# Optimization experiments

Hardware: AMD Instinct MI355X
Metric: run time of the kernel (lower is better)

Reference implementation:

```python
import jax, jax.numpy as jnp
import numpy as np
from jax import lax


def _conv(x, w, b):
    # NCHW valid conv, stride 1 (torch Conv2d semantics)
    y = lax.conv_general_dilated(x, w, (1, 1), 'VALID',
                                 dimension_numbers=('NCHW', 'OIHW', 'NCHW'))
    return y + b[None, :, None, None]


def _maxpool(x, k, s):
    return lax.reduce_window(x, -jnp.inf, lax.max, (1, 1, k, k), (1, 1, s, s), 'VALID')


def _lin(x, w, b):
    # torch nn.Linear: y = x @ W^T + b, applied to last dim
    return x @ w.T + b


def setup_inputs() -> dict:
    key = jax.random.key(0)
    ks = jax.random.split(key, 21)
    def f(i, shape, scale):
        return jax.random.normal(ks[i], shape, dtype=jnp.float32) * scale
    return {
        'x': f(0, (512, 1, 28, 28), 1.0),
        'c1_w': f(1, (50, 1, 3, 3), 0.33), 'c1_b': f(2, (50,), 0.1),
        'c2_w': f(3, (50, 50, 3, 3), 0.047), 'c2_b': f(4, (50,), 0.05),
        'c3_w': f(5, (50, 50, 3, 3), 0.047), 'c3_b': f(6, (50,), 0.05),
        'l1_w': f(7, (500, 50), 0.14), 'l1_b': f(8, (500,), 0.05),
        'l2_w': f(9, (10, 500), 0.045), 'l2_b': f(10, (10,), 0.05),
        'd1_w': f(11, (3, 8450), 0.011), 'd1_b': f(12, (3,), 0.05),
        'd2_w': f(13, (2, 1250), 0.028), 'd2_b': f(14, (2,), 0.05),
        'c1c3_w': f(15, (13, 13), 0.28), 'c1c3_b': f(16, (13,), 0.05),
        'c1l1_w': f(17, (500, 1), 1.0), 'c1l1_b': f(18, (500,), 0.05),
        'c2l1_w': f(19, (500, 5), 0.45), 'c2l1_b': f(20, (500,), 0.05),
    }


def reference(x, c1_w, c1_b, c2_w, c2_b, c3_w, c3_b, l1_w, l1_b, l2_w, l2_b,
              d1_w, d1_b, d2_w, d2_b, c1c3_w, c1c3_b, c1l1_w, c1l1_b,
              c2l1_w, c2l1_b):
    B = x.shape[0]
    # stage 1: conv1 + relu + pool2 -> [B,50,13,13]
    h1 = _maxpool(jax.nn.relu(_conv(x, c1_w, c1_b)), 2, 2)
    # router 1 (argmax over 3 branches): 0 -> conv2 path, 1 -> c1_c3 path, 2 -> early-exit linear path
    d1 = jnp.argmax(_lin(h1.reshape(B, -1), d1_w, d1_b), axis=1)  # [B]
    # branch l11 (d1==2): pool7 -> [B,50,1,1], Linear(1->500) on last dim -> [B,50,1,500]
    l11 = _lin(_maxpool(h1, 7, 7), c1l1_w, c1l1_b)
    # branch c3-direct (d1==1): Linear(13->13) on last dim, then conv3+relu+pool2 -> [B,50,5,5]
    c33 = _lin(h1, c1c3_w, c1c3_b)
    c3d = _maxpool(jax.nn.relu(_conv(c33, c3_w, c3_b)), 2, 2)
    # branch c2 (d1==0): conv2+relu+pool2 -> [B,50,5,5]
    h2 = _maxpool(jax.nn.relu(_conv(h1, c2_w, c2_b)), 2, 2)
    # router 2 (argmax over 2 sub-branches)
    d2 = jnp.argmax(_lin(h2.reshape(B, -1), d2_w, d2_b), axis=1)  # [B]
    # sub-branch c32 (d2==0): conv3+relu+pool2 -> [B,50,1,1]
    c32 = _maxpool(jax.nn.relu(_conv(h2, c3_w, c3_b)), 2, 2)
    # sub-branch l12 (d2==1): Linear(5->500) on last dim -> [B,50,5,500], pool3 -> [B,50,1,166]
    l12 = _maxpool(_lin(h2, c2l1_w, c2l1_b), 3, 3)

    def head(t):
        # original: .view(-1, 50) -> linear1/relu/linear2/log_softmax; row-major flatten per sample
        r = t.reshape(B, -1, 50)
        return jax.nn.log_softmax(_lin(jax.nn.relu(_lin(r, l1_w, l1_b)), l2_w, l2_b), axis=-1)

    dt = x.dtype
    m_l11 = (d1 == 2).astype(dt)[:, None, None]
    m_c3d = (d1 == 1).astype(dt)[:, None, None]
    m_c32 = ((d1 == 0) & (d2 == 0)).astype(dt)[:, None, None]
    m_l12 = ((d1 == 0) & (d2 == 1)).astype(dt)[:, None, None]
    # dense masked combine (static-shape equivalent of the gather/compute/concat dispatch);
    # branch order matches the original concatenation: l11, l12, c32, c3-direct
    out = jnp.concatenate([head(l11) * m_l11, head(l12) * m_l12,
                           head(c32) * m_c32, head(c3d) * m_c3d], axis=1)  # [B,692,10]
    return out, d1, d2
```

## Files before the change

kernel.cpp:

```cpp
#include <hip/hip_runtime.h>
#include <hip/hip_bf16.h>
#include <math.h>

#define BB 512
#define CC 50

typedef __attribute__((ext_vector_type(8))) __bf16 bf16x8;
typedef __attribute__((ext_vector_type(4))) float f32x4;

__global__ void k_zero(float* __restrict__ out, int n4) {
  int i = blockIdx.x * 256 + threadIdx.x;
  if (i < n4) {
    float4 z = {0.f, 0.f, 0.f, 0.f};
    ((float4*)out)[i] = z;
  }
}

__global__ void k_pack(const float* __restrict__ l1w, const float* __restrict__ l1b,
                       const float* __restrict__ l2w,
                       __bf16* __restrict__ W1p, __bf16* __restrict__ W2p) {
  int idx = blockIdx.x * 256 + threadIdx.x;
  if (idx < 512 * 64) {
    int j = idx >> 6, k = idx & 63;
    float v = 0.f;
    if (j < 500) {
      if (k < 50) v = l1w[j * 50 + k];
      else if (k == 50) v = l1b[j];
    }
    W1p[idx] = (__bf16)v;
  } else if (idx < 512 * 64 + 16 * 512) {
    int i2 = idx - 512 * 64;
    int n = i2 >> 9, k2 = i2 & 511;
    float v = (n < 10 && k2 < 500) ? l2w[n * 500 + k2] : 0.f;
    W2p[i2] = (__bf16)v;
  }
}

__global__ void k_conv1(const float* __restrict__ x, const float* __restrict__ w,
                        const float* __restrict__ bias, float* __restrict__ h1) {
  int idx = blockIdx.x * 256 + threadIdx.x;
  if (idx >= BB * CC * 169) return;
  int b = idx / (CC * 169);
  int rem = idx % (CC * 169);
  int c = rem / 169;
  int p = rem % 169;
  int py = p / 13, px = p % 13;
  const float* xi = x + b * 784;
  float wr[9];
#pragma unroll
  for (int i = 0; i < 9; i++) wr[i] = w[c * 9 + i];
  float m = -INFINITY;
#pragma unroll
  for (int dy = 0; dy < 2; dy++)
#pragma unroll
    for (int dx = 0; dx < 2; dx++) {
      int y0 = 2 * py + dy, x0 = 2 * px + dx;
      float s = 0.f;
#pragma unroll
      for (int ky = 0; ky < 3; ky++)
#pragma unroll
        for (int kx = 0; kx < 3; kx++)
          s += xi[(y0 + ky) * 28 + x0 + kx] * wr[ky * 3 + kx];
      m = fmaxf(m, s);
    }
  h1[idx] = fmaxf(m + bias[c], 0.f);
}

__global__ void k_d1p7(const float* __restrict__ h1, const float* __restrict__ w,
                       const float* __restrict__ bias, int* __restrict__ d1i,
                       float* __restrict__ outd1, float* __restrict__ p7) {
  int b = blockIdx.x, t = threadIdx.x;
  const float* hb = h1 + b * 8450;
  float s0 = 0.f, s1 = 0.f, s2 = 0.f;
  for (int i = t; i < 8450; i += 256) {
    float v = hb[i];
    s0 += v * w[i];
    s1 += v * w[8450 + i];
    s2 += v * w[16900 + i];
  }
#pragma unroll
  for (int off = 32; off >= 1; off >>= 1) {
    s0 += __shfl_down(s0, off);
    s1 += __shfl_down(s1, off);
    s2 += __shfl_down(s2, off);
  }
  __shared__ float red[4][3];
  if ((t & 63) == 0) { red[t >> 6][0] = s0; red[t >> 6][1] = s1; red[t >> 6][2] = s2; }
  __syncthreads();
  if (t == 0) {
    float l0 = bias[0], l1v = bias[1], l2v = bias[2];
    for (int wv = 0; wv < 4; wv++) { l0 += red[wv][0]; l1v += red[wv][1]; l2v += red[wv][2]; }
    int idx = 0; float best = l0;
    if (l1v > best) { best = l1v; idx = 1; }
    if (l2v > best) { best = l2v; idx = 2; }
    d1i[b] = idx;
    outd1[b] = (float)idx;
  }
  if (t < 50) {
    const float* hp = hb + t * 169;
    float m = -INFINITY;
#pragma unroll
    for (int y = 0; y < 7; y++)
#pragma unroll
      for (int x = 0; x < 7; x++) m = fmaxf(m, hp[y * 13 + x]);
    p7[b * 50 + t] = m;
  }
}

template <int MODE>
__global__ __launch_bounds__(256) void k_conv5(const float* __restrict__ in,
                                               const float* __restrict__ w,
                                               const float* __restrict__ bias,
                                               const int* __restrict__ d1i,
                                               const float* __restrict__ w13,
                                               const float* __restrict__ b13,
                                               float* __restrict__ out) {
  int b = blockIdx.x;
  if (MODE == 1 && d1i[b] != 1) return;
  __shared__ float sh[50 * 260];
  __shared__ float w13s[182];
  int t = threadIdx.x;
  for (int i = t; i < 8450; i += 256) {
    int ic = i / 169, r = i % 169;
    int row = r / 13, xx = r % 13;
    sh[ic * 260 + row * 20 + xx] = in[b * 8450 + i];
  }
  if (MODE == 1) {
    for (int i = t; i < 182; i += 256) w13s[i] = (i < 169) ? w13[i] : b13[i - 169];
  }
  __syncthreads();
  if (MODE == 1) {
    for (int p = t; p < 650; p += 256) {
      float* row = sh + (p / 13) * 260 + (p % 13) * 20;
      float r[13];
#pragma unroll
      for (int k = 0; k < 13; k++) r[k] = row[k];
#pragma unroll
      for (int xx = 0; xx < 13; xx++) {
        float s = w13s[169 + xx];
#pragma unroll
        for (int k = 0; k < 13; k++) s += r[k] * w13s[xx * 13 + k];
        row[xx] = s;
      }
    }
    __syncthreads();
  }
  if (t >= 250) return;
  int oc = t / 5, py = t % 5;
  float acc[5][4];
#pragma unroll
  for (int i = 0; i < 5; i++)
#pragma unroll
    for (int j = 0; j < 4; j++) acc[i][j] = 0.f;
  const float* wb = w + oc * 450;
  for (int ic = 0; ic < 50; ic++) {
    float wv[9];
#pragma unroll
    for (int i = 0; i < 9; i++) wv[i] = wb[ic * 9 + i];
    float r[4][13];
    const float* rp = sh + ic * 260 + 2 * py * 20;
#pragma unroll
    for (int rr = 0; rr < 4; rr++) {
      const float* p4 = rp + rr * 20;
      float4 q0 = *(const float4*)(p4);
      float4 q1 = *(const float4*)(p4 + 4);
      float4 q2 = *(const float4*)(p4 + 8);
      r[rr][0] = q0.x; r[rr][1] = q0.y; r[rr][2] = q0.z; r[rr][3] = q0.w;
      r[rr][4] = q1.x; r[rr][5] = q1.y; r[rr][6] = q1.z; r[rr][7] = q1.w;
      r[rr][8] = q2.x; r[rr][9] = q2.y; r[rr][10] = q2.z; r[rr][11] = q2.w;
      r[rr][12] = p4[12];
    }
#pragma unroll
    for (int px = 0; px < 5; px++)
#pragma unroll
      for (int dy = 0; dy < 2; dy++)
#pragma unroll
        for (int dx = 0; dx < 2; dx++) {
          float s = acc[px][dy * 2 + dx];
          int x0 = 2 * px + dx;
#pragma unroll
          for (int ky = 0; ky < 3; ky++)
#pragma unroll
            for (int kx = 0; kx < 3; kx++)
              s += r[dy + ky][x0 + kx] * wv[ky * 3 + kx];
          acc[px][dy * 2 + dx] = s;
        }
  }
  float bs = bias[oc];
#pragma unroll
  for (int px = 0; px < 5; px++) {
    float m = fmaxf(fmaxf(acc[px][0], acc[px][1]), fmaxf(acc[px][2], acc[px][3]));
    out[((b * 50 + oc) * 5 + py) * 5 + px] = fmaxf(m + bs, 0.f);
  }
}

__global__ __launch_bounds__(256) void k_d2c(const float* __restrict__ h2,
                                             const float* __restrict__ d2w,
                                             const float* __restrict__ d2b,
                                             const float* __restrict__ c3w,
                                             const float* __restrict__ c3b,
                                             const float* __restrict__ c2l1w,
                                             const float* __restrict__ c2l1b,
                                             const int* __restrict__ d1i,
                                             int* __restrict__ d2i,
                                             float* __restrict__ outd2,
                                             float* __restrict__ c32,
                                             float* __restrict__ l12) {
  int b = blockIdx.x, t = threadIdx.x;
  __shared__ float hs[1250];
  __shared__ float wls[2500];
  __shared__ float bls[500];
  __shared__ float red[4][2];
  __shared__ int sd2;
  for (int i = t; i < 1250; i += 256) hs[i] = h2[b * 1250 + i];
  __syncthreads();
  float s0 = 0.f, s1 = 0.f;
  for (int i = t; i < 1250; i += 256) {
    float v = hs[i];
    s0 += v * d2w[i];
    s1 += v * d2w[1250 + i];
  }
#pragma unroll
  for (int off = 32; off >= 1; off >>= 1) {
    s0 += __shfl_down(s0, off);
    s1 += __shfl_down(s1, off);
  }
  if ((t & 63) == 0) { red[t >> 6][0] = s0; red[t >> 6][1] = s1; }
  __syncthreads();
  if (t == 0) {
    float l0 = d2b[0] + red[0][0] + red[1][0] + red[2][0] + red[3][0];
    float l1v = d2b[1] + red[0][1] + red[1][1] + red[2][1] + red[3][1];
    int idx = (l1v > l0) ? 1 : 0;
    d2i[b] = idx;
    outd2[b] = (float)idx;
    sd2 = idx;
  }
  __syncthreads();
  int d2v = sd2;
  if (d1i[b] != 0) return;
  if (d2v == 0) {
    if (t < 50) {
      const float* wb = c3w + t * 450;
      float a[4] = {0.f, 0.f, 0.f, 0.f};
      for (int ic = 0; ic < 50; ic++) {
        float r[4][4];
#pragma unroll
        for (int y = 0; y < 4; y++)
#pragma unroll
          for (int xx = 0; xx < 4; xx++) r[y][xx] = hs[ic * 25 + y * 5 + xx];
        float wv[9];
#pragma unroll
        for (int i = 0; i < 9; i++) wv[i] = wb[ic * 9 + i];
#pragma unroll
        for (int py = 0; py < 2; py++)
#pragma unroll
          for (int px = 0; px < 2; px++) {
            float s = a[py * 2 + px];
#pragma unroll
            for (int ky = 0; ky < 3; ky++)
#pragma unroll
              for (int kx = 0; kx < 3; kx++)
                s += r[py + ky][px + kx] * wv[ky * 3 + kx];
            a[py * 2 + px] = s;
          }
      }
      float m = fmaxf(fmaxf(a[0], a[1]), fmaxf(a[2], a[3]));
      c32[b * 50 + t] = fmaxf(m + c3b[t], 0.f);
    }
  } else {
    for (int i = t; i < 2500; i += 256) wls[i] = c2l1w[i];
    for (int i = t; i < 500; i += 256) bls[i] = c2l1b[i];
    __syncthreads();
    for (int o = t; o < 8300; o += 256) {
      int c = o / 166, tt = o % 166;
      const float* hb = hs + c * 25;
      float m = -INFINITY;
#pragma unroll
      for (int i = 0; i < 3; i++) {
        float a0 = hb[i * 5 + 0], a1 = hb[i * 5 + 1], a2 = hb[i * 5 + 2],
              a3 = hb[i * 5 + 3], a4 = hb[i * 5 + 4];
#pragma unroll
        for (int dj = 0; dj < 3; dj++) {
          int j = 3 * tt + dj;
          const float* wj = wls + j * 5;
          float s = bls[j] + a0 * wj[0] + a1 * wj[1] + a2 * wj[2] + a3 * wj[3] + a4 * wj[4];
          m = fmaxf(m, s);
        }
      }
      l12[b * 8300 + o] = m;
    }
  }
}

__device__ __forceinline__ int swz(int byteoff) {
  return byteoff ^ (((byteoff >> 7) & 7) << 4);
}

__global__ __launch_bounds__(256) void k_head(
    const float* __restrict__ h2, const float* __restrict__ c3d,
    const float* __restrict__ c32, const float* __restrict__ p7,
    const float* __restrict__ l12buf,
    const int* __restrict__ d1i, const int* __restrict__ d2i,
    const __bf16* __restrict__ W1p, const __bf16* __restrict__ W2p,
    const float* __restrict__ l2b,
    const float* __restrict__ c1l1w, const float* __restrict__ c1l1b,
    float* __restrict__ out) {
  int b = blockIdx.x >> 1;
  int half = blockIdx.x & 1;
  int d1 = d1i[b], d2 = d2i[b];
  int branch, nrows, rstart;
  if (d1 == 2)      { branch = 0; nrows = 500; rstart = 0; }
  else if (d1 == 1) { branch = 3; nrows = 25;  rstart = 667; }
  else if (d2 == 1) { branch = 1; nrows = 166; rstart = 500; }
  else              { branch = 2; nrows = 1;   rstart = 666; }
  int base = half * 256;
  if (base >= nrows) return;
  int nr = nrows - base; if (nr > 256) nr = 256;

  __shared__ __align__(16) char smem[53248];
  __bf16* Vs = (__bf16*)smem;
  char* Wst = smem;
  __bf16* Ht = (__bf16*)(smem + 32768);
  int t = threadIdx.x;

  for (int idx = t; idx < 256 * 64; idx += 256) {
    int row = idx >> 6, col = idx & 63;
    float val = 0.f;
    if (col == 50) val = 1.0f;
    else if (col < 50 && row < nr) {
      int rr = base + row;
      if (branch == 0) {
        int c = rr / 10; int j = (rr % 10) * 50 + col;
        val = p7[b * 50 + c] * c1l1w[j] + c1l1b[j];
      } else if (branch == 1) {
        val = l12buf[b * 8300 + rr * 50 + col];
      } else if (branch == 2) {
        val = c32[b * 50 + col];
      } else {
        int k = rr * 50 + col; int c = k / 25, s5 = k % 25;
        val = c3d[(b * 50 + c) * 25 + s5];
      }
    }
    Vs[row * 72 + col] = (__bf16)val;
  }

  bf16x8 st[4];
  {
    const __bf16* s0 = W1p + t * 32;
#pragma unroll
    for (int i = 0; i < 4; ++i) st[i] = *(const bf16x8*)(s0 + i * 8);
  }
  __syncthreads();

  int wv = t >> 6, lane = t & 63;
  int lr = lane & 15, lg = lane >> 4;
  int wbase = wv * 64;
  bool active = wbase < nr;
  int wrem = active ? (nr - wbase) : 0;
  int nmt = (wrem + 15) >> 4; if (nmt > 4) nmt = 4;

  bf16x8 a1[4][2];
  if (active) {
#pragma unroll
    for (int mt = 0; mt < 4; ++mt) {
      if (mt < nmt) {
#pragma unroll
        for (int ks = 0; ks < 2; ++ks)
          a1[mt][ks] = *(const bf16x8*)(Vs + (wbase + mt * 16 + lr) * 72 + ks * 32 + lg * 8);
      }
    }
  }
  __syncthreads();

  {
#pragma unroll
    for (int i = 0; i < 4; ++i)
      *(bf16x8*)(Wst + swz(t * 64 + i * 16)) = st[i];
  }
  __syncthreads();

  const __bf16* w2b = W2p + lr * 512 + lg * 8;
  f32x4 acc2[4];
#pragma unroll
  for (int mt = 0; mt < 4; ++mt) acc2[mt] = (f32x4){0.f, 0.f, 0.f, 0.f};
  bf16x8 b2n = *(const bf16x8*)(w2b);

  for (int c = 0; c < 4; ++c) {
    if (c < 3) {
      const __bf16* s2 = W1p + (c + 1) * 8192 + t * 32;
#pragma unroll
      for (int i = 0; i < 4; ++i) st[i] = *(const bf16x8*)(s2 + i * 8);
    }
    char* wb = Wst + (c & 1) * 16384;
    if (active) {
#pragma unroll
      for (int ql = 0; ql < 4; ++ql) {
        int q = c * 4 + ql;
        int boff = ql * 4096 + lr * 128 + lg * 16;
        bf16x8 bA0 = *(const bf16x8*)(wb + swz(boff));
        bf16x8 bA1 = *(const bf16x8*)(wb + swz(boff + 64));
        bf16x8 bB0 = *(const bf16x8*)(wb + swz(boff + 2048));
        bf16x8 bB1 = *(const bf16x8*)(wb + swz(boff + 2048 + 64));
#pragma unroll
        for (int mt = 0; mt < 4; ++mt) {
          if (mt < nmt) {
            f32x4 dz = {0.f, 0.f, 0.f, 0.f};
            f32x4 d = __builtin_amdgcn_mfma_f32_16x16x32_bf16(a1[mt][0], bA0, dz, 0, 0, 0);
            d = __builtin_amdgcn_mfma_f32_16x16x32_bf16(a1[mt][1], bA1, d, 0, 0, 0);
            __bf16* hp = Ht + (wv * 4 + mt) * 640;
#pragma unroll
            for (int r = 0; r < 4; ++r)
              hp[(lg * 4 + r) * 40 + lr] = (__bf16)fmaxf(d[r], 0.f);
          }
        }
#pragma unroll
        for (int mt = 0; mt < 4; ++mt) {
          if (mt < nmt) {
            f32x4 dz = {0.f, 0.f, 0.f, 0.f};
            f32x4 d = __builtin_amdgcn_mfma_f32_16x16x32_bf16(a1[mt][0], bB0, dz, 0, 0, 0);
            d = __builtin_amdgcn_mfma_f32_16x16x32_bf16(a1[mt][1], bB1, d, 0, 0, 0);
            __bf16* hp = Ht + (wv * 4 + mt) * 640;
#pragma unroll
            for (int r = 0; r < 4; ++r)
              hp[(lg * 4 + r) * 40 + 16 + lr] = (__bf16)fmaxf(d[r], 0.f);
          }
        }
        {
          bf16x8 bb2 = b2n;
          if (q < 15) b2n = *(const bf16x8*)(w2b + (q + 1) * 32);
#pragma unroll
          for (int mt = 0; mt < 4; ++mt) {
            if (mt < nmt) {
              bf16x8 a2 = *(const bf16x8*)(Ht + (wv * 4 + mt) * 640 + lr * 40 + lg * 8);
              acc2[mt] = __builtin_amdgcn_mfma_f32_16x16x32_bf16(a2, bb2, acc2[mt], 0, 0, 0);
            }
          }
        }
      }
    }
    if (c < 3) {
      char* wd = Wst + (1 - (c & 1)) * 16384;
#pragma unroll
      for (int i = 0; i < 4; ++i)
        *(bf16x8*)(wd + swz(t * 64 + i * 16)) = st[i];
    }
    __syncthreads();
  }
  if (!active) return;

  float bl = (lr < 10) ? l2b[lr] : 0.f;
#pragma unroll
  for (int mt = 0; mt < 4; ++mt) {
    if (mt < nmt) {
      float o[4], m[4], s[4];
#pragma unroll
      for (int r = 0; r < 4; ++r) {
        o[r] = acc2[mt][r] + bl;
        m[r] = (lr < 10) ? o[r] : -INFINITY;
      }
#pragma unroll
      for (int mk = 1; mk < 16; mk <<= 1)
#pragma unroll
        for (int r = 0; r < 4; ++r) m[r] = fmaxf(m[r], __shfl_xor(m[r], mk));
#pragma unroll
      for (int r = 0; r < 4; ++r) s[r] = (lr < 10) ? expf(o[r] - m[r]) : 0.f;
#pragma unroll
      for (int mk = 1; mk < 16; mk <<= 1)
#pragma unroll
        for (int r = 0; r < 4; ++r) s[r] += __shfl_xor(s[r], mk);
      if (lr < 10) {
#pragma unroll
        for (int r = 0; r < 4; ++r) {
          int rloc = wbase + mt * 16 + lg * 4 + r;
          if (rloc < nr)
            out[(b * 692 + rstart + base + rloc) * 10 + lr] = o[r] - (m[r] + logf(s[r]));
        }
      }
    }
  }
}

extern "C" void kernel_launch(void* const* d_in, const int* in_sizes, int n_in,
                              void* d_out, int out_size, void* d_ws, size_t ws_size,
                              hipStream_t stream) {
  const float* x     = (const float*)d_in[0];
  const float* c1w   = (const float*)d_in[1];
  const float* c1b   = (const float*)d_in[2];
  const float* c2w   = (const float*)d_in[3];
  const float* c2b   = (const float*)d_in[4];
  const float* c3w   = (const float*)d_in[5];
  const float* c3b   = (const float*)d_in[6];
  const float* l1w   = (const float*)d_in[7];
  const float* l1b   = (const float*)d_in[8];
  const float* l2w   = (const float*)d_in[9];
  const float* l2b   = (const float*)d_in[10];
  const float* d1w   = (const float*)d_in[11];
  const float* d1b   = (const float*)d_in[12];
  const float* d2w   = (const float*)d_in[13];
  const float* d2b   = (const float*)d_in[14];
  const float* c13w  = (const float*)d_in[15];
  const float* c13b  = (const float*)d_in[16];
  const float* c1l1w = (const float*)d_in[17];
  const float* c1l1b = (const float*)d_in[18];
  const float* c2l1w = (const float*)d_in[19];
  const float* c2l1b = (const float*)d_in[20];
  float* out = (float*)d_out;

  float* ws  = (float*)d_ws;
  float* h1  = ws;
  float* h2  = h1 + 4326400;
  float* c3d = h2 + 640000;
  float* c32 = c3d + 640000;
  float* p7  = c32 + 25600;
  int*   d1i = (int*)(p7 + 25600);
  int*   d2i = d1i + 512;
  __bf16* W1p = (__bf16*)(d2i + 512);
  __bf16* W2p = W1p + 512 * 64;
  float* l12buf = h1;

  float* outd1 = out + 512 * 692 * 10;
  float* outd2 = outd1 + 512;

  k_zero<<<3460, 256, 0, stream>>>(out, 885510);
  k_pack<<<160, 256, 0, stream>>>(l1w, l1b, l2w, W1p, W2p);
  k_conv1<<<16900, 256, 0, stream>>>(x, c1w, c1b, h1);
  k_d1p7<<<512, 256, 0, stream>>>(h1, d1w, d1b, d1i, outd1, p7);
  k_conv5<0><<<512, 256, 0, stream>>>(h1, c2w, c2b, d1i, c13w, c13b, h2);
  k_conv5<1><<<512, 256, 0, stream>>>(h1, c3w, c3b, d1i, c13w, c13b, c3d);
  k_d2c<<<512, 256, 0, stream>>>(h2, d2w, d2b, c3w, c3b, c2l1w, c2l1b,
                                 d1i, d2i, outd2, c32, l12buf);
  k_head<<<1024, 256, 0, stream>>>(h2, c3d, c32, p7, l12buf, d1i, d2i,
                                   W1p, W2p, l2b, c1l1w, c1l1b, out);
}
```

Before: 237.2 us.

## Replace LDS-staged head GEMM with register-only MFMA plus scalar FP32 second layer

The head kernel no longer stages activations and W1 tiles through shared memory with barriers and swizzling. Each wave loads its A fragments directly from global memory and streams W1 fragments from global/L2 with a two-deep register prefetch. The second linear layer (500->10) is now done as FP32 FMAs against a transposed W2 table, followed by a cross-lane shuffle reduction. The grid is split into four 128-row slabs per sample instead of two 256-row halves, so waves with no rows exit early. This removes LDS traffic and synchronization but adds many VALU FMAs, a large register accumulator array (80 floats), and 40 shuffle reductions per row tile.

```diff
diff --git a/kernel.cpp b/kernel.cpp
--- a/kernel.cpp
+++ b/kernel.cpp
@@ -18,7 +18,7 @@
 
 __global__ void k_pack(const float* __restrict__ l1w, const float* __restrict__ l1b,
                        const float* __restrict__ l2w,
-                       __bf16* __restrict__ W1p, __bf16* __restrict__ W2p) {
+                       __bf16* __restrict__ W1p, float* __restrict__ W2t) {
   int idx = blockIdx.x * 256 + threadIdx.x;
   if (idx < 512 * 64) {
     int j = idx >> 6, k = idx & 63;
@@ -28,11 +28,10 @@
       else if (k == 50) v = l1b[j];
     }
     W1p[idx] = (__bf16)v;
-  } else if (idx < 512 * 64 + 16 * 512) {
+  } else if (idx < 512 * 64 + 512 * 12) {
     int i2 = idx - 512 * 64;
-    int n = i2 >> 9, k2 = i2 & 511;
-    float v = (n < 10 && k2 < 500) ? l2w[n * 500 + k2] : 0.f;
-    W2p[i2] = (__bf16)v;
+    int j = i2 / 12, n = i2 % 12;
+    W2t[i2] = (n < 10 && j < 500) ? l2w[n * 500 + j] : 0.f;
   }
 }
 
@@ -292,188 +291,172 @@
   }
 }
 
-__device__ __forceinline__ int swz(int byteoff) {
-  return byteoff ^ (((byteoff >> 7) & 7) << 4);
-}
-
-__global__ __launch_bounds__(256) void k_head(
-    const float* __restrict__ h2, const float* __restrict__ c3d,
-    const float* __restrict__ c32, const float* __restrict__ p7,
-    const float* __restrict__ l12buf,
+__global__ __launch_bounds__(256) void k_gemm(
+    const float* __restrict__ c3d, const float* __restrict__ c32,
+    const float* __restrict__ p7, const float* __restrict__ l12buf,
     const int* __restrict__ d1i, const int* __restrict__ d2i,
-    const __bf16* __restrict__ W1p, const __bf16* __restrict__ W2p,
+    const __bf16* __restrict__ W1p, const float* __restrict__ W2t,
     const float* __restrict__ l2b,
     const float* __restrict__ c1l1w, const float* __restrict__ c1l1b,
     float* __restrict__ out) {
-  int b = blockIdx.x >> 1;
-  int half = blockIdx.x & 1;
+  int b = blockIdx.x >> 2;
+  int slab = blockIdx.x & 3;
   int d1 = d1i[b], d2 = d2i[b];
   int branch, nrows, rstart;
   if (d1 == 2)      { branch = 0; nrows = 500; rstart = 0; }
   else if (d1 == 1) { branch = 3; nrows = 25;  rstart = 667; }
   else if (d2 == 1) { branch = 1; nrows = 166; rstart = 500; }
   else              { branch = 2; nrows = 1;   rstart = 666; }
-  int base = half * 256;
-  if (base >= nrows) return;
-  int nr = nrows - base; if (nr > 256) nr = 256;
-
-  __shared__ __align__(16) char smem[53248];
-  __bf16* Vs = (__bf16*)smem;
-  char* Wst = smem;
-  __bf16* Ht = (__bf16*)(smem + 32768);
+
   int t = threadIdx.x;
-
-  for (int idx = t; idx < 256 * 64; idx += 256) {
-    int row = idx >> 6, col = idx & 63;
-    float val = 0.f;
-    if (col == 50) val = 1.0f;
-    else if (col < 50 && row < nr) {
-      int rr = base + row;
-      if (branch == 0) {
-        int c = rr / 10; int j = (rr % 10) * 50 + col;
-        val = p7[b * 50 + c] * c1l1w[j] + c1l1b[j];
-      } else if (branch == 1) {
-        val = l12buf[b * 8300 + rr * 50 + col];
-      } else if (branch == 2) {
-        val = c32[b * 50 + col];
-      } else {
-        int k = rr * 50 + col; int c = k / 25, s5 = k % 25;
-        val = c3d[(b * 50 + c) * 25 + s5];
-      }
-    }
-    Vs[row * 72 + col] = (__bf16)val;
-  }
-
-  bf16x8 st[4];
-  {
-    const __bf16* s0 = W1p + t * 32;
-#pragma unroll
-    for (int i = 0; i < 4; ++i) st[i] = *(const bf16x8*)(s0 + i * 8);
-  }
-  __syncthreads();
-
   int wv = t >> 6, lane = t & 63;
   int lr = lane & 15, lg = lane >> 4;
-  int wbase = wv * 64;
-  bool active = wbase < nr;
-  int wrem = active ? (nr - wbase) : 0;
-  int nmt = (wrem + 15) >> 4; if (nmt > 4) nmt = 4;
-
-  bf16x8 a1[4][2];
-  if (active) {
-#pragma unroll
-    for (int mt = 0; mt < 4; ++mt) {
+  int rowbase = slab * 128 + wv * 32;
+  if (rowbase >= nrows) return;
+  int rem = nrows - rowbase;
+  int nmt = (rem + 15) >> 4; if (nmt > 2) nmt = 2;
+
+  bf16x8 a1[2][2];
+#pragma unroll
+  for (int mt = 0; mt < 2; ++mt) {
+    int m = rowbase + mt * 16 + lr;
+    const float* src;
+    float p7v = 0.f; const float* wsrc = nullptr; const float* bsrc = nullptr;
+    if (branch == 0) {
+      p7v = p7[b * 50 + m / 10];
+      wsrc = c1l1w + (m % 10) * 50;
+      bsrc = c1l1b + (m % 10) * 50;
+      src = wsrc;
+    } else if (branch == 1) {
+      src = l12buf + b * 8300 + m * 50;
+    } else if (branch == 2) {
+      src = c32 + b * 50 + m * 50;
+    } else {
+      src = c3d + b * 1250 + m * 50;
+    }
+#pragma unroll
+    for (int ks = 0; ks < 2; ++ks) {
+      float v[8];
+      int k0 = ks * 32 + lg * 8;
+      if (ks == 0 || lg < 2) {
+        if (branch == 0) {
+#pragma unroll
+          for (int i = 0; i < 8; i += 2) {
+            float2 wq = *(const float2*)(wsrc + k0 + i);
+            float2 bq = *(const float2*)(bsrc + k0 + i);
+            v[i] = p7v * wq.x + bq.x;
+            v[i + 1] = p7v * wq.y + bq.y;
+          }
+        } else {
+#pragma unroll
+          for (int i = 0; i < 8; i += 2) {
+            float2 q = *(const float2*)(src + k0 + i);
+            v[i] = q.x; v[i + 1] = q.y;
+          }
+        }
+      } else if (lg == 2) {
+        float2 q;
+        if (branch == 0) {
+          float2 wq = *(const float2*)(wsrc + 48);
+          float2 bq = *(const float2*)(bsrc + 48);
+          q.x = p7v * wq.x + bq.x; q.y = p7v * wq.y + bq.y;
+        } else {
+          q = *(const float2*)(src + 48);
+        }
+        v[0] = q.x; v[1] = q.y; v[2] = 1.0f;
+        v[3] = 0.f; v[4] = 0.f; v[5] = 0.f; v[6] = 0.f; v[7] = 0.f;
+      } else {
+#pragma unroll
+        for (int i = 0; i < 8; ++i) v[i] = 0.f;
+      }
+      bf16x8 a;
+#pragma unroll
+      for (int i = 0; i < 8; ++i) a[i] = (__bf16)v[i];
+      a1[mt][ks] = a;
+    }
+  }
+
+  const __bf16* w1b = W1p + lr * 64 + lg * 8;
+  float acc[2][4][10];
+#pragma unroll
+  for (int mt = 0; mt < 2; ++mt)
+#pragma unroll
+    for (int r = 0; r < 4; ++r)
+#pragma unroll
+      for (int n = 0; n < 10; ++n) acc[mt][r][n] = 0.f;
+
+  bf16x8 c0a = *(const bf16x8*)(w1b);
+  bf16x8 c0b = *(const bf16x8*)(w1b + 32);
+  bf16x8 c1a = *(const bf16x8*)(w1b + 1024);
+  bf16x8 c1b = *(const bf16x8*)(w1b + 1024 + 32);
+
+  for (int jt = 0; jt < 32; ++jt) {
+    bf16x8 b0 = c0a, b1 = c0b;
+    c0a = c1a; c0b = c1b;
+    if (jt + 2 < 32) {
+      c1a = *(const bf16x8*)(w1b + (jt + 2) * 1024);
+      c1b = *(const bf16x8*)(w1b + (jt + 2) * 1024 + 32);
+    }
+    const float* wr = W2t + (jt * 16 + lr) * 12;
+    float4 w20 = *(const float4*)(wr);
+    float4 w21 = *(const float4*)(wr + 4);
+    float2 w22 = *(const float2*)(wr + 8);
+    float w2v[10] = {w20.x, w20.y, w20.z, w20.w, w21.x, w21.y, w21.z, w21.w, w22.x, w22.y};
+#pragma unroll
+    for (int mt = 0; mt < 2; ++mt) {
       if (mt < nmt) {
-#pragma unroll
-        for (int ks = 0; ks < 2; ++ks)
-          a1[mt][ks] = *(const bf16x8*)(Vs + (wbase + mt * 16 + lr) * 72 + ks * 32 + lg * 8);
+        f32x4 dz = {0.f, 0.f, 0.f, 0.f};
+        f32x4 h = __builtin_amdgcn_mfma_f32_16x16x32_bf16(a1[mt][0], b0, dz, 0, 0, 0);
+        h = __builtin_amdgcn_mfma_f32_16x16x32_bf16(a1[mt][1], b1, h, 0, 0, 0);
+#pragma unroll
+        for (int r = 0; r < 4; ++r) {
+          float hv = fmaxf(h[r], 0.f);
+#pragma unroll
+          for (int n = 0; n < 10; ++n) acc[mt][r][n] += hv * w2v[n];
+        }
       }
     }
   }
-  __syncthreads();
-
-  {
-#pragma unroll
-    for (int i = 0; i < 4; ++i)
-      *(bf16x8*)(Wst + swz(t * 64 + i * 16)) = st[i];
-  }
-  __syncthreads();
-
-  const __bf16* w2b = W2p + lr * 512 + lg * 8;
-  f32x4 acc2[4];
-#pragma unroll
-  for (int mt = 0; mt < 4; ++mt) acc2[mt] = (f32x4){0.f, 0.f, 0.f, 0.f};
-  bf16x8 b2n = *(const bf16x8*)(w2b);
-
-  for (int c = 0; c < 4; ++c) {
-    if (c < 3) {
-      const __bf16* s2 = W1p + (c + 1) * 8192 + t * 32;
-#pragma unroll
-      for (int i = 0; i < 4; ++i) st[i] = *(const bf16x8*)(s2 + i * 8);
-    }
-    char* wb = Wst + (c & 1) * 16384;
-    if (active) {
-#pragma unroll
-      for (int ql = 0; ql < 4; ++ql) {
-        int q = c * 4 + ql;
-        int boff = ql * 4096 + lr * 128 + lg * 16;
-        bf16x8 bA0 = *(const bf16x8*)(wb + swz(boff));
-        bf16x8 bA1 = *(const bf16x8*)(wb + swz(boff + 64));
-        bf16x8 bB0 = *(const bf16x8*)(wb + swz(boff + 2048));
-        bf16x8 bB1 = *(const bf16x8*)(wb + swz(boff + 2048 + 64));
-#pragma unroll
-        for (int mt = 0; mt < 4; ++mt) {
-          if (mt < nmt) {
-            f32x4 dz = {0.f, 0.f, 0.f, 0.f};
-            f32x4 d = __builtin_amdgcn_mfma_f32_16x16x32_bf16(a1[mt][0], bA0, dz, 0, 0, 0);
-            d = __builtin_amdgcn_mfma_f32_16x16x32_bf16(a1[mt][1], bA1, d, 0, 0, 0);
-            __bf16* hp = Ht + (wv * 4 + mt) * 640;
-#pragma unroll
-            for (int r = 0; r < 4; ++r)
-              hp[(lg * 4 + r) * 40 + lr] = (__bf16)fmaxf(d[r], 0.f);
+
+#pragma unroll
+  for (int mt = 0; mt < 2; ++mt) {
+    if (mt < nmt) {
+#pragma unroll
+      for (int r = 0; r < 4; ++r)
+#pragma unroll
+        for (int n = 0; n < 10; ++n) {
+          float v = acc[mt][r][n];
+          v += __shfl_xor(v, 1);
+          v += __shfl_xor(v, 2);
+          v += __shfl_xor(v, 4);
+          v += __shfl_xor(v, 8);
+          acc[mt][r][n] = v;
+        }
+    }
+  }
+  if (lr == 0) {
+#pragma unroll
+    for (int mt = 0; mt < 2; ++mt) {
+      if (mt < nmt) {
+#pragma unroll
+        for (int r = 0; r < 4; ++r) {
+          int row = rowbase + mt * 16 + lg * 4 + r;
+          if (row < nrows) {
+            float o[10];
+            float m = -INFINITY;
+#pragma unroll
+            for (int n = 0; n < 10; ++n) {
+              o[n] = acc[mt][r][n] + l2b[n];
+              m = fmaxf(m, o[n]);
+            }
+            float s = 0.f;
+#pragma unroll
+            for (int n = 0; n < 10; ++n) s += expf(o[n] - m);
+            float lse = m + logf(s);
+            float* orow = out + (b * 692 + rstart + row) * 10;
+#pragma unroll
+            for (int n = 0; n < 10; ++n) orow[n] = o[n] - lse;
           }
-        }
-#pragma unroll
-        for (int mt = 0; mt < 4; ++mt) {
-          if (mt < nmt) {
-            f32x4 dz = {0.f, 0.f, 0.f, 0.f};
-            f32x4 d = __builtin_amdgcn_mfma_f32_16x16x32_bf16(a1[mt][0], bB0, dz, 0, 0, 0);
-            d = __builtin_amdgcn_mfma_f32_16x16x32_bf16(a1[mt][1], bB1, d, 0, 0, 0);
-            __bf16* hp = Ht + (wv * 4 + mt) * 640;
-#pragma unroll
-            for (int r = 0; r < 4; ++r)
-              hp[(lg * 4 + r) * 40 + 16 + lr] = (__bf16)fmaxf(d[r], 0.f);
-          }
-        }
-        {
-          bf16x8 bb2 = b2n;
-          if (q < 15) b2n = *(const bf16x8*)(w2b + (q + 1) * 32);
-#pragma unroll
-          for (int mt = 0; mt < 4; ++mt) {
-            if (mt < nmt) {
-              bf16x8 a2 = *(const bf16x8*)(Ht + (wv * 4 + mt) * 640 + lr * 40 + lg * 8);
-              acc2[mt] = __builtin_amdgcn_mfma_f32_16x16x32_bf16(a2, bb2, acc2[mt], 0, 0, 0);
-            }
-          }
-        }
-      }
-    }
-    if (c < 3) {
-      char* wd = Wst + (1 - (c & 1)) * 16384;
-#pragma unroll
-      for (int i = 0; i < 4; ++i)
-        *(bf16x8*)(wd + swz(t * 64 + i * 16)) = st[i];
-    }
-    __syncthreads();
-  }
-  if (!active) return;
-
-  float bl = (lr < 10) ? l2b[lr] : 0.f;
-#pragma unroll
-  for (int mt = 0; mt < 4; ++mt) {
-    if (mt < nmt) {
-      float o[4], m[4], s[4];
-#pragma unroll
-      for (int r = 0; r < 4; ++r) {
-        o[r] = acc2[mt][r] + bl;
-        m[r] = (lr < 10) ? o[r] : -INFINITY;
-      }
-#pragma unroll
-      for (int mk = 1; mk < 16; mk <<= 1)
-#pragma unroll
-        for (int r = 0; r < 4; ++r) m[r] = fmaxf(m[r], __shfl_xor(m[r], mk));
-#pragma unroll
-      for (int r = 0; r < 4; ++r) s[r] = (lr < 10) ? expf(o[r] - m[r]) : 0.f;
-#pragma unroll
-      for (int mk = 1; mk < 16; mk <<= 1)
-#pragma unroll
-        for (int r = 0; r < 4; ++r) s[r] += __shfl_xor(s[r], mk);
-      if (lr < 10) {
-#pragma unroll
-        for (int r = 0; r < 4; ++r) {
-          int rloc = wbase + mt * 16 + lg * 4 + r;
-          if (rloc < nr)
-            out[(b * 692 + rstart + base + rloc) * 10 + lr] = o[r] - (m[r] + logf(s[r]));
         }
       }
     }
@@ -515,20 +498,20 @@
   int*   d1i = (int*)(p7 + 25600);
   int*   d2i = d1i + 512;
   __bf16* W1p = (__bf16*)(d2i + 512);
-  __bf16* W2p = W1p + 512 * 64;
+  float* W2t = (float*)(W1p + 512 * 64);
   float* l12buf = h1;
 
   float* outd1 = out + 512 * 692 * 10;
   float* outd2 = outd1 + 512;
 
   k_zero<<<3460, 256, 0, stream>>>(out, 885510);
-  k_pack<<<160, 256, 0, stream>>>(l1w, l1b, l2w, W1p, W2p);
+  k_pack<<<153, 256, 0, stream>>>(l1w, l1b, l2w, W1p, W2t);
   k_conv1<<<16900, 256, 0, stream>>>(x, c1w, c1b, h1);
   k_d1p7<<<512, 256, 0, stream>>>(h1, d1w, d1b, d1i, outd1, p7);
   k_conv5<0><<<512, 256, 0, stream>>>(h1, c2w, c2b, d1i, c13w, c13b, h2);
   k_conv5<1><<<512, 256, 0, stream>>>(h1, c3w, c3b, d1i, c13w, c13b, c3d);
   k_d2c<<<512, 256, 0, stream>>>(h2, d2w, d2b, c3w, c3b, c2l1w, c2l1b,
                                  d1i, d2i, outd2, c32, l12buf);
-  k_head<<<1024, 256, 0, stream>>>(h2, c3d, c32, p7, l12buf, d1i, d2i,
-                                   W1p, W2p, l2b, c1l1w, c1l1b, out);
-}
+  k_gemm<<<2048, 256, 0, stream>>>(c3d, c32, p7, l12buf, d1i, d2i,
+                                   W1p, W2t, l2b, c1l1w, c1l1b, out);
+}
```

Result: slower. 276.7 us (+16.7%).
